# Optimization experiments

Measured on AMD Instinct MI355X. Metric: run time of the kernel, lower is better.

The kernel has to match this reference:

```python
import jax, jax.numpy as jnp
import numpy as np


def setup_inputs() -> dict:
    key = jax.random.key(0)
    kx, ky = jax.random.split(key)
    B, N, M, D = 8, 4096, 4096, 128
    x = jax.random.normal(kx, (B, N, D), dtype=jnp.float32)
    y = jax.random.normal(ky, (B, M, D), dtype=jnp.float32)
    return {"x": x, "y": y}


def reference(x, y):
    # Pairwise L2 distances, equivalent to torch.cdist(x, y) (p=2).
    # ||x_i - y_j||^2 = ||x_i||^2 + ||y_j||^2 - 2 <x_i, y_j>
    x2 = jnp.sum(x * x, axis=-1)[:, :, None]          # [B, N, 1]
    y2 = jnp.sum(y * y, axis=-1)[:, None, :]          # [B, 1, M]
    xy = jnp.einsum("bnd,bmd->bnm", x, y)             # [B, N, M]
    D = jnp.sqrt(jnp.maximum(x2 + y2 - 2.0 * xy, 0.0))  # [B, N, M]
    coverage = D.min(axis=1).mean(axis=-1)            # min over N -> [B, M] -> [B]
    precision = D.min(axis=2).mean(axis=-1)           # min over M -> [B, N] -> [B]
    return (coverage + precision).mean()              # scalar Chamfer loss
```

## Files before the change

kernel.cpp:

```cpp
#include <hip/hip_runtime.h>
#include <cstdint>


#define B_   8
#define N_   4096
#define M_   4096
#define D_   128
#define TPB  8
#define ROWS_PB 256
#define XG   (N_ / ROWS_PB)
#define CHUNKS (M_ / (TPB * 64))

typedef __bf16 bf16x8 __attribute__((ext_vector_type(8)));
typedef float  f32x4  __attribute__((ext_vector_type(4)));
typedef unsigned int u32;

static __device__ __forceinline__ unsigned short f2bf(float f) {
  unsigned u = __float_as_uint(f);
  u += 0x7FFFu + ((u >> 16) & 1u);
  return (unsigned short)(u >> 16);
}

static __device__ __forceinline__ void gld16(void* lds, const void* g) {
  __builtin_amdgcn_global_load_lds(
      (const __attribute__((address_space(1))) void*)g,
      (__attribute__((address_space(3))) void*)lds, 16, 0, 0);
}

__global__ __launch_bounds__(256) void pass1_prep(
    const float* __restrict__ x, const float* __restrict__ y,
    unsigned short* __restrict__ xb, unsigned short* __restrict__ yb,
    float* __restrict__ x2, float* __restrict__ y2)
{
  const int ROWS = B_ * N_;
  int gw   = (blockIdx.x * 256 + threadIdx.x) >> 6;
  int lane = threadIdx.x & 63;
  int half = lane >> 5, sub = lane & 31;
  int row2 = gw * 2 + half;
  bool isx = row2 < ROWS;
  const float* src; unsigned short* dst; float* nrm; int row;
  if (isx) { src = x; dst = xb; nrm = x2; row = row2; }
  else     { src = y; dst = yb; nrm = y2; row = row2 - ROWS; }
  size_t base = (size_t)row * D_ + sub * 4;
  float4 v = *(const float4*)(src + base);
  float sx = isx ? -2.0f : 1.0f;
  u32 p0 = (u32)f2bf(sx * v.x) | ((u32)f2bf(sx * v.y) << 16);
  u32 p1 = (u32)f2bf(sx * v.z) | ((u32)f2bf(sx * v.w) << 16);
  *(uint2*)(dst + base) = make_uint2(p0, p1);
  float s = v.x * v.x + v.y * v.y + v.z * v.z + v.w * v.w;
  #pragma unroll
  for (int m = 1; m < 32; m <<= 1) s += __shfl_xor(s, m, 64);
  if (sub == 0) nrm[row] = s;
}

__global__ __launch_bounds__(256) void pass2_tile(
    const unsigned short* __restrict__ xb, const unsigned short* __restrict__ yb,
    const float* __restrict__ x2, const float* __restrict__ y2,
    float* __restrict__ rowpart, float* __restrict__ colpart)
{
  __shared__ unsigned short ys[2 * 8192];
  __shared__ float cminW[2][16 * 64];

  const int tid  = threadIdx.x;
  const int wave = tid >> 6;
  const int lane = tid & 63;
  const int quad = lane >> 4;
  const int l15  = lane & 15;

  const int id    = blockIdx.x;
  const int b     = id & 7;
  const int xg    = (id >> 3) & 15;
  const int chunk = id >> 7;
  const int n0    = xg * ROWS_PB;
  const int mc0   = chunk * (TPB * 64);

  int srcoff[4], ldsoff[4];
  #pragma unroll
  for (int i = 0; i < 4; ++i) {
    int p  = (wave * 4 + i) * 1024 + lane * 16;
    int r  = p >> 8;
    int pc = (p >> 4) & 15;
    int c  = pc ^ (r & 15);
    srcoff[i] = r * D_ + c * 8;
    ldsoff[i] = (wave * 4 + i) * 1024;
  }

  {
    const unsigned short* src = yb + ((size_t)b * M_ + mc0) * D_;
    #pragma unroll
    for (int i = 0; i < 4; ++i) gld16((char*)ys + ldsoff[i], src + srcoff[i]);
  }

  bf16x8 afrag[4][4];
  const size_t xrow0 = (size_t)b * N_ + n0 + wave * 64;
  #pragma unroll
  for (int kb = 0; kb < 4; ++kb)
    #pragma unroll
    for (int rt = 0; rt < 4; ++rt)
      afrag[kb][rt] = *(const bf16x8*)(xb + (xrow0 + rt * 16 + l15) * D_ + kb * 32 + quad * 8);

  f32x4 xvv[4];
  #pragma unroll
  for (int rt = 0; rt < 4; ++rt)
    #pragma unroll
    for (int r = 0; r < 4; ++r)
      xvv[rt][r] = x2[(size_t)b * N_ + n0 + wave * 64 + rt * 16 + quad * 4 + r];

  const float FINF = __uint_as_float(0x7F800000u);
  float rmin2[4][4];
  #pragma unroll
  for (int rt = 0; rt < 4; ++rt)
    #pragma unroll
    for (int r = 0; r < 4; ++r) rmin2[rt][r] = FINF;

  #pragma unroll 1
  for (int t = 0; t < TPB; ++t) {
    const int m0 = mc0 + t * 64;
    const int d  = (t & 1) * 16384;
    __syncthreads();

    float y2r[4];
    #pragma unroll
    for (int ct = 0; ct < 4; ++ct)
      y2r[ct] = y2[(size_t)b * M_ + m0 + ct * 16 + l15];

    if (t + 1 < TPB) {
      const unsigned short* src = yb + ((size_t)b * M_ + m0 + 64) * D_;
      char* dst = (char*)ys + (16384 - d);
      #pragma unroll
      for (int i = 0; i < 4; ++i) gld16(dst + ldsoff[i], src + srcoff[i]);
    }

    if (t > 0 && tid < 64) {
      const float* cb = cminW[(t - 1) & 1];
      float v = cb[tid];
      #pragma unroll
      for (int w = 1; w < 16; ++w) v = fminf(v, cb[w * 64 + tid]);
      colpart[(size_t)xg * (B_ * M_) + (size_t)b * M_ + (m0 - 64) + tid] = v;
    }

    #pragma unroll
    for (int ct = 0; ct < 4; ++ct) {
      f32x4 a[4];
      #pragma unroll
      for (int rt = 0; rt < 4; ++rt) a[rt] = xvv[rt];
      #pragma unroll
      for (int kb = 0; kb < 4; ++kb) {
        const int row = ct * 16 + l15;
        const int pcB = (kb * 4 + quad) ^ l15;
        bf16x8 bfr = *(const bf16x8*)((const char*)ys + d + row * 256 + pcB * 16);
        #pragma unroll
        for (int rt = 0; rt < 4; ++rt)
          a[rt] = __builtin_amdgcn_mfma_f32_16x16x32_bf16(afrag[kb][rt], bfr, a[rt], 0, 0, 0);
      }
      float yv = y2r[ct];
      float cm = FINF;
      #pragma unroll
      for (int rt = 0; rt < 4; ++rt) {
        #pragma unroll
        for (int r = 0; r < 4; ++r) {
          float s = a[rt][r] + yv;
          rmin2[rt][r] = fminf(rmin2[rt][r], s);
          cm = fminf(cm, s);
        }
      }
      cminW[t & 1][(wave * 4 + quad) * 64 + ct * 16 + l15] = cm;
    }
  }

  __syncthreads();
  if (tid < 64) {
    const float* cb = cminW[(TPB - 1) & 1];
    float v = cb[tid];
    #pragma unroll
    for (int w = 1; w < 16; ++w) v = fminf(v, cb[w * 64 + tid]);
    colpart[(size_t)xg * (B_ * M_) + (size_t)b * M_ + (mc0 + (TPB - 1) * 64) + tid] = v;
  }

  #pragma unroll
  for (int rt = 0; rt < 4; ++rt) {
    #pragma unroll
    for (int r = 0; r < 4; ++r) {
      float v = rmin2[rt][r];
      v = fminf(v, __shfl_xor(v, 1, 64));
      v = fminf(v, __shfl_xor(v, 2, 64));
      v = fminf(v, __shfl_xor(v, 4, 64));
      v = fminf(v, __shfl_xor(v, 8, 64));
      if (l15 == 0)
        rowpart[(size_t)chunk * (B_ * N_) + (size_t)b * N_ + n0 + wave * 64 + rt * 16 + quad * 4 + r] = v;
    }
  }
}

__global__ __launch_bounds__(256) void pass3_final(
    const float* __restrict__ rowpart, const float* __restrict__ colpart,
    float* __restrict__ out)
{
  const int BN = B_ * N_;
  float s1 = 0.0f, s2 = 0.0f;
  for (int i = blockIdx.x * 256 + threadIdx.x; i < BN; i += 64 * 256) {
    float r = rowpart[i];
    #pragma unroll
    for (int c = 1; c < CHUNKS; ++c) r = fminf(r, rowpart[c * BN + i]);
    s1 += sqrtf(fmaxf(r, 0.0f));
    float m = colpart[i];
    #pragma unroll
    for (int g = 1; g < XG; ++g) m = fminf(m, colpart[g * BN + i]);
    s2 += sqrtf(fmaxf(m, 0.0f));
  }
  float s = s1 + s2;
  #pragma unroll
  for (int m = 1; m < 64; m <<= 1) s += __shfl_xor(s, m, 64);
  __shared__ float r1[4];
  int wave = threadIdx.x >> 6, lane = threadIdx.x & 63;
  if (lane == 0) r1[wave] = s;
  __syncthreads();
  if (threadIdx.x == 0)
    atomicAdd(out, (r1[0] + r1[1] + r1[2] + r1[3]) / (float)(B_ * N_));
}

extern "C" void kernel_launch(void* const* d_in, const int* in_sizes, int n_in,
                              void* d_out, int out_size, void* d_ws, size_t ws_size,
                              hipStream_t stream)
{
  const float* x = (const float*)d_in[0];
  const float* y = (const float*)d_in[1];
  char* ws = (char*)d_ws;

  unsigned short* xb = (unsigned short*)(ws);
  unsigned short* yb = (unsigned short*)(ws + (8u << 20));
  float* x2      = (float*)(ws + (16u << 20));
  float* y2      = (float*)(ws + (16u << 20) + (1u << 17));
  float* rowpart = (float*)(ws + (16u << 20) + (2u << 17));
  float* colpart = (float*)(ws + (16u << 20) + (10u << 17));
  float* outf = (float*)d_out;

  hipMemsetAsync(outf, 0, sizeof(float), stream);

  pass1_prep<<<(B_ * N_) / 4, 256, 0, stream>>>(x, y, xb, yb, x2, y2);

  pass2_tile<<<B_ * XG * CHUNKS, 256, 0, stream>>>(xb, yb, x2, y2, rowpart, colpart);

  pass3_final<<<64, 256, 0, stream>>>(rowpart, colpart, outf);
}
```

Baseline: 121.6 us.

## Replace partial-min buffers with global atomicMin and drop LDS column reduction

The row and column minima are now reduced straight into global arrays using integer atomicMin on the float bit patterns. The arrays are initialised to +inf in the prep pass. This removes the LDS cross-wave column-min buffer and its per-tile reduction, and shrinks the final pass from scanning 8 and 16 partial slices down to a single pass. The B fragment loads are also batched ahead of the MFMA block, which is wrapped in s_setprio. The cost is many contended global atomics per column, up to 64 writers per address.

```diff
diff --git a/kernel.cpp b/kernel.cpp
--- a/kernel.cpp
+++ b/kernel.cpp
@@ -30,7 +30,8 @@
 __global__ __launch_bounds__(256) void pass1_prep(
     const float* __restrict__ x, const float* __restrict__ y,
     unsigned short* __restrict__ xb, unsigned short* __restrict__ yb,
-    float* __restrict__ x2, float* __restrict__ y2)
+    float* __restrict__ x2, float* __restrict__ y2,
+    float* __restrict__ rowmin, float* __restrict__ colmin)
 {
   const int ROWS = B_ * N_;
   int gw   = (blockIdx.x * 256 + threadIdx.x) >> 6;
@@ -38,9 +39,9 @@
   int half = lane >> 5, sub = lane & 31;
   int row2 = gw * 2 + half;
   bool isx = row2 < ROWS;
-  const float* src; unsigned short* dst; float* nrm; int row;
-  if (isx) { src = x; dst = xb; nrm = x2; row = row2; }
-  else     { src = y; dst = yb; nrm = y2; row = row2 - ROWS; }
+  const float* src; unsigned short* dst; float* nrm; float* minp; int row;
+  if (isx) { src = x; dst = xb; nrm = x2; minp = rowmin; row = row2; }
+  else     { src = y; dst = yb; nrm = y2; minp = colmin; row = row2 - ROWS; }
   size_t base = (size_t)row * D_ + sub * 4;
   float4 v = *(const float4*)(src + base);
   float sx = isx ? -2.0f : 1.0f;
@@ -50,16 +51,16 @@
   float s = v.x * v.x + v.y * v.y + v.z * v.z + v.w * v.w;
   #pragma unroll
   for (int m = 1; m < 32; m <<= 1) s += __shfl_xor(s, m, 64);
-  if (sub == 0) nrm[row] = s;
+  if (sub == 0)      nrm[row]  = s;
+  else if (sub == 1) minp[row] = __uint_as_float(0x7F800000u);
 }
 
 __global__ __launch_bounds__(256) void pass2_tile(
     const unsigned short* __restrict__ xb, const unsigned short* __restrict__ yb,
     const float* __restrict__ x2, const float* __restrict__ y2,
-    float* __restrict__ rowpart, float* __restrict__ colpart)
+    float* __restrict__ rowmin, float* __restrict__ colmin)
 {
   __shared__ unsigned short ys[2 * 8192];
-  __shared__ float cminW[2][16 * 64];
 
   const int tid  = threadIdx.x;
   const int wave = tid >> 6;
@@ -119,11 +120,6 @@
     const int d  = (t & 1) * 16384;
     __syncthreads();
 
-    float y2r[4];
-    #pragma unroll
-    for (int ct = 0; ct < 4; ++ct)
-      y2r[ct] = y2[(size_t)b * M_ + m0 + ct * 16 + l15];
-
     if (t + 1 < TPB) {
       const unsigned short* src = yb + ((size_t)b * M_ + m0 + 64) * D_;
       char* dst = (char*)ys + (16384 - d);
@@ -131,50 +127,48 @@
       for (int i = 0; i < 4; ++i) gld16(dst + ldsoff[i], src + srcoff[i]);
     }
 
-    if (t > 0 && tid < 64) {
-      const float* cb = cminW[(t - 1) & 1];
-      float v = cb[tid];
-      #pragma unroll
-      for (int w = 1; w < 16; ++w) v = fminf(v, cb[w * 64 + tid]);
-      colpart[(size_t)xg * (B_ * M_) + (size_t)b * M_ + (m0 - 64) + tid] = v;
-    }
+    float y2r[4];
+    #pragma unroll
+    for (int ct = 0; ct < 4; ++ct)
+      y2r[ct] = y2[(size_t)b * M_ + m0 + ct * 16 + l15];
 
     #pragma unroll
     for (int ct = 0; ct < 4; ++ct) {
-      f32x4 a[4];
-      #pragma unroll
-      for (int rt = 0; rt < 4; ++rt) a[rt] = xvv[rt];
+      bf16x8 bfr[4];
       #pragma unroll
       for (int kb = 0; kb < 4; ++kb) {
         const int row = ct * 16 + l15;
         const int pcB = (kb * 4 + quad) ^ l15;
-        bf16x8 bfr = *(const bf16x8*)((const char*)ys + d + row * 256 + pcB * 16);
+        bfr[kb] = *(const bf16x8*)((const char*)ys + d + row * 256 + pcB * 16);
+      }
+      f32x4 a[4];
+      #pragma unroll
+      for (int rt = 0; rt < 4; ++rt) a[rt] = xvv[rt];
+      __builtin_amdgcn_s_setprio(1);
+      #pragma unroll
+      for (int kb = 0; kb < 4; ++kb)
         #pragma unroll
         for (int rt = 0; rt < 4; ++rt)
-          a[rt] = __builtin_amdgcn_mfma_f32_16x16x32_bf16(afrag[kb][rt], bfr, a[rt], 0, 0, 0);
+          a[rt] = __builtin_amdgcn_mfma_f32_16x16x32_bf16(afrag[kb][rt], bfr[kb], a[rt], 0, 0, 0);
+      __builtin_amdgcn_s_setprio(0);
+
+      float yv = y2r[ct];
+      float c[4];
+      #pragma unroll
+      for (int rt = 0; rt < 4; ++rt) {
+        float s0 = a[rt][0] + yv; rmin2[rt][0] = fminf(rmin2[rt][0], s0);
+        float s1 = a[rt][1] + yv; rmin2[rt][1] = fminf(rmin2[rt][1], s1);
+        float s2 = a[rt][2] + yv; rmin2[rt][2] = fminf(rmin2[rt][2], s2);
+        float s3 = a[rt][3] + yv; rmin2[rt][3] = fminf(rmin2[rt][3], s3);
+        c[rt] = fminf(fminf(s0, s1), fminf(s2, s3));
       }
-      float yv = y2r[ct];
-      float cm = FINF;
-      #pragma unroll
-      for (int rt = 0; rt < 4; ++rt) {
-        #pragma unroll
-        for (int r = 0; r < 4; ++r) {
-          float s = a[rt][r] + yv;
-          rmin2[rt][r] = fminf(rmin2[rt][r], s);
-          cm = fminf(cm, s);
-        }
-      }
-      cminW[t & 1][(wave * 4 + quad) * 64 + ct * 16 + l15] = cm;
+      float cm = fminf(fminf(c[0], c[1]), fminf(c[2], c[3]));
+      cm = fminf(cm, __shfl_xor(cm, 16, 64));
+      cm = fminf(cm, __shfl_xor(cm, 32, 64));
+      if (quad == 0)
+        atomicMin((int*)(colmin + (size_t)b * M_ + m0 + ct * 16 + l15),
+                  __float_as_int(cm));
     }
-  }
-
-  __syncthreads();
-  if (tid < 64) {
-    const float* cb = cminW[(TPB - 1) & 1];
-    float v = cb[tid];
-    #pragma unroll
-    for (int w = 1; w < 16; ++w) v = fminf(v, cb[w * 64 + tid]);
-    colpart[(size_t)xg * (B_ * M_) + (size_t)b * M_ + (mc0 + (TPB - 1) * 64) + tid] = v;
   }
 
   #pragma unroll
@@ -187,26 +181,21 @@
       v = fminf(v, __shfl_xor(v, 4, 64));
       v = fminf(v, __shfl_xor(v, 8, 64));
       if (l15 == 0)
-        rowpart[(size_t)chunk * (B_ * N_) + (size_t)b * N_ + n0 + wave * 64 + rt * 16 + quad * 4 + r] = v;
+        atomicMin((int*)(rowmin + (size_t)b * N_ + n0 + wave * 64 + rt * 16 + quad * 4 + r),
+                  __float_as_int(v));
     }
   }
 }
 
 __global__ __launch_bounds__(256) void pass3_final(
-    const float* __restrict__ rowpart, const float* __restrict__ colpart,
+    const float* __restrict__ rowmin, const float* __restrict__ colmin,
     float* __restrict__ out)
 {
   const int BN = B_ * N_;
   float s1 = 0.0f, s2 = 0.0f;
   for (int i = blockIdx.x * 256 + threadIdx.x; i < BN; i += 64 * 256) {
-    float r = rowpart[i];
-    #pragma unroll
-    for (int c = 1; c < CHUNKS; ++c) r = fminf(r, rowpart[c * BN + i]);
-    s1 += sqrtf(fmaxf(r, 0.0f));
-    float m = colpart[i];
-    #pragma unroll
-    for (int g = 1; g < XG; ++g) m = fminf(m, colpart[g * BN + i]);
-    s2 += sqrtf(fmaxf(m, 0.0f));
+    s1 += sqrtf(fmaxf(rowmin[i], 0.0f));
+    s2 += sqrtf(fmaxf(colmin[i], 0.0f));
   }
   float s = s1 + s2;
   #pragma unroll
@@ -229,17 +218,17 @@
 
   unsigned short* xb = (unsigned short*)(ws);
   unsigned short* yb = (unsigned short*)(ws + (8u << 20));
-  float* x2      = (float*)(ws + (16u << 20));
-  float* y2      = (float*)(ws + (16u << 20) + (1u << 17));
-  float* rowpart = (float*)(ws + (16u << 20) + (2u << 17));
-  float* colpart = (float*)(ws + (16u << 20) + (10u << 17));
+  float* x2     = (float*)(ws + (16u << 20));
+  float* y2     = (float*)(ws + (16u << 20) + (1u << 17));
+  float* rowmin = (float*)(ws + (16u << 20) + (2u << 17));
+  float* colmin = (float*)(ws + (16u << 20) + (3u << 17));
   float* outf = (float*)d_out;
 
   hipMemsetAsync(outf, 0, sizeof(float), stream);
 
-  pass1_prep<<<(B_ * N_) / 4, 256, 0, stream>>>(x, y, xb, yb, x2, y2);
-
-  pass2_tile<<<B_ * XG * CHUNKS, 256, 0, stream>>>(xb, yb, x2, y2, rowpart, colpart);
-
-  pass3_final<<<64, 256, 0, stream>>>(rowpart, colpart, outf);
-}
+  pass1_prep<<<(B_ * N_) / 4, 256, 0, stream>>>(x, y, xb, yb, x2, y2, rowmin, colmin);
+
+  pass2_tile<<<B_ * XG * CHUNKS, 256, 0, stream>>>(xb, yb, x2, y2, rowmin, colmin);
+
+  pass3_final<<<64, 256, 0, stream>>>(rowmin, colmin, outf);
+}
```

New measurement: 127.6 us. 1.05x slower.

## Fuse bf16 conversion and norm computation into tile kernel, drop prep pass

Applied to the files above, without the earlier changes.

Removes the separate prep kernel. The tile kernel now loads fp32 x and y directly, converts them to bf16 in registers, computes the squared norms on the fly, and writes the y tiles into swizzled LDS. The next y tile is prefetched through registers in two halves interleaved between MFMA column tiles, replacing the global_load_lds path. Column-min partials are pre-reduced with a shuffle, which halves the cminW reduction. This removes one launch and the bf16 workspace round trip, but each x row block and y chunk is now converted redundantly by many blocks, and more VALU and register work sits inside the main loop.

```diff
diff --git a/kernel.cpp b/kernel.cpp
--- a/kernel.cpp
+++ b/kernel.cpp
@@ -10,6 +10,7 @@
 #define ROWS_PB 256
 #define XG   (N_ / ROWS_PB)
 #define CHUNKS (M_ / (TPB * 64))
+#define GRID (B_ * XG * CHUNKS)
 
 typedef __bf16 bf16x8 __attribute__((ext_vector_type(8)));
 typedef float  f32x4  __attribute__((ext_vector_type(4)));
@@ -20,52 +21,56 @@
   u += 0x7FFFu + ((u >> 16) & 1u);
   return (unsigned short)(u >> 16);
 }
-
-static __device__ __forceinline__ void gld16(void* lds, const void* g) {
-  __builtin_amdgcn_global_load_lds(
-      (const __attribute__((address_space(1))) void*)g,
-      (__attribute__((address_space(3))) void*)lds, 16, 0, 0);
-}
-
-__global__ __launch_bounds__(256) void pass1_prep(
+static __device__ __forceinline__ u32 pk2(float a, float b) {
+  return (u32)f2bf(a) | ((u32)f2bf(b) << 16);
+}
+
+
+#define DO_CT(CT)                                                              \
+  {                                                                            \
+    f32x4 a[4];                                                                \
+    _Pragma("unroll")                                                          \
+    for (int rt = 0; rt < 4; ++rt) a[rt] = xvv[rt];                            \
+    _Pragma("unroll")                                                          \
+    for (int kb = 0; kb < 4; ++kb) {                                           \
+      const int row = (CT) * 16 + l15;                                         \
+      const int pcB = (kb * 4 + quad) ^ l15;                                   \
+      bf16x8 bfr = *(const bf16x8*)((const char*)ys + d + row * 256 + pcB * 16); \
+      _Pragma("unroll")                                                        \
+      for (int rt = 0; rt < 4; ++rt)                                           \
+        a[rt] = __builtin_amdgcn_mfma_f32_16x16x32_bf16(afrag[kb][rt], bfr, a[rt], 0, 0, 0); \
+    }                                                                          \
+    float yv = y2r[(CT)];                                                      \
+    float cm = FINF;                                                           \
+    _Pragma("unroll")                                                          \
+    for (int rt = 0; rt < 4; ++rt) {                                           \
+      _Pragma("unroll")                                                        \
+      for (int r = 0; r < 4; ++r) {                                            \
+        float s = a[rt][r] + yv;                                               \
+        rmin2[rt][r] = fminf(rmin2[rt][r], s);                                 \
+        cm = fminf(cm, s);                                                     \
+      }                                                                        \
+    }                                                                          \
+    cm = fminf(cm, __shfl_xor(cm, 16, 64));               \
+    if ((quad & 1) == 0)                                                       \
+      cminW[t & 1][wave * 2 + (quad >> 1)][(CT) * 16 + l15] = cm;              \
+  }
+
+__global__ __launch_bounds__(256) void tile_fused(
     const float* __restrict__ x, const float* __restrict__ y,
-    unsigned short* __restrict__ xb, unsigned short* __restrict__ yb,
-    float* __restrict__ x2, float* __restrict__ y2)
-{
-  const int ROWS = B_ * N_;
-  int gw   = (blockIdx.x * 256 + threadIdx.x) >> 6;
-  int lane = threadIdx.x & 63;
-  int half = lane >> 5, sub = lane & 31;
-  int row2 = gw * 2 + half;
-  bool isx = row2 < ROWS;
-  const float* src; unsigned short* dst; float* nrm; int row;
-  if (isx) { src = x; dst = xb; nrm = x2; row = row2; }
-  else     { src = y; dst = yb; nrm = y2; row = row2 - ROWS; }
-  size_t base = (size_t)row * D_ + sub * 4;
-  float4 v = *(const float4*)(src + base);
-  float sx = isx ? -2.0f : 1.0f;
-  u32 p0 = (u32)f2bf(sx * v.x) | ((u32)f2bf(sx * v.y) << 16);
-  u32 p1 = (u32)f2bf(sx * v.z) | ((u32)f2bf(sx * v.w) << 16);
-  *(uint2*)(dst + base) = make_uint2(p0, p1);
-  float s = v.x * v.x + v.y * v.y + v.z * v.z + v.w * v.w;
-  #pragma unroll
-  for (int m = 1; m < 32; m <<= 1) s += __shfl_xor(s, m, 64);
-  if (sub == 0) nrm[row] = s;
-}
-
-__global__ __launch_bounds__(256) void pass2_tile(
-    const unsigned short* __restrict__ xb, const unsigned short* __restrict__ yb,
-    const float* __restrict__ x2, const float* __restrict__ y2,
     float* __restrict__ rowpart, float* __restrict__ colpart)
 {
   __shared__ unsigned short ys[2 * 8192];
-  __shared__ float cminW[2][16 * 64];
+  __shared__ float ys2[2][64];
+  __shared__ float cminW[2][8][64];
 
   const int tid  = threadIdx.x;
   const int wave = tid >> 6;
   const int lane = tid & 63;
   const int quad = lane >> 4;
   const int l15  = lane & 15;
+  const int r0   = tid >> 2;
+  const int qp   = tid & 3;
 
   const int id    = blockIdx.x;
   const int b     = id & 7;
@@ -74,37 +79,61 @@
   const int n0    = xg * ROWS_PB;
   const int mc0   = chunk * (TPB * 64);
 
-  int srcoff[4], ldsoff[4];
-  #pragma unroll
-  for (int i = 0; i < 4; ++i) {
-    int p  = (wave * 4 + i) * 1024 + lane * 16;
-    int r  = p >> 8;
-    int pc = (p >> 4) & 15;
-    int c  = pc ^ (r & 15);
-    srcoff[i] = r * D_ + c * 8;
-    ldsoff[i] = (wave * 4 + i) * 1024;
-  }
-
   {
-    const unsigned short* src = yb + ((size_t)b * M_ + mc0) * D_;
-    #pragma unroll
-    for (int i = 0; i < 4; ++i) gld16((char*)ys + ldsoff[i], src + srcoff[i]);
+    const float* ysrc = y + (size_t)(b * M_ + mc0 + r0) * D_ + qp * 32;
+    float4 v0[8];
+    #pragma unroll
+    for (int i = 0; i < 8; ++i) v0[i] = *(const float4*)(ysrc + i * 4);
+    float p = 0.0f;
+    #pragma unroll
+    for (int i = 0; i < 8; ++i)
+      p += v0[i].x*v0[i].x + v0[i].y*v0[i].y + v0[i].z*v0[i].z + v0[i].w*v0[i].w;
+    p += __shfl_xor(p, 1, 64);
+    p += __shfl_xor(p, 2, 64);
+    if ((lane & 3) == 0) ys2[0][r0] = p;
+    #pragma unroll
+    for (int j = 0; j < 4; ++j) {
+      int pc = (qp * 4 + j) ^ (r0 & 15);
+      uint4 w;
+      w.x = pk2(v0[2*j].x,   v0[2*j].y);
+      w.y = pk2(v0[2*j].z,   v0[2*j].w);
+      w.z = pk2(v0[2*j+1].x, v0[2*j+1].y);
+      w.w = pk2(v0[2*j+1].z, v0[2*j+1].w);
+      *(uint4*)((char*)ys + r0 * 256 + pc * 16) = w;
+    }
   }
 
   bf16x8 afrag[4][4];
-  const size_t xrow0 = (size_t)b * N_ + n0 + wave * 64;
-  #pragma unroll
-  for (int kb = 0; kb < 4; ++kb)
+  f32x4 xvv[4];
+  {
+    float x2row[4];
+    #pragma unroll
+    for (int rt = 0; rt < 4; ++rt) {
+      const float* xs = x + (size_t)(b * N_ + n0 + wave * 64 + rt * 16 + l15) * D_ + quad * 8;
+      float p = 0.0f;
+      #pragma unroll
+      for (int kb = 0; kb < 4; ++kb) {
+        float4 u0 = *(const float4*)(xs + kb * 32);
+        float4 u1 = *(const float4*)(xs + kb * 32 + 4);
+        p += u0.x*u0.x + u0.y*u0.y + u0.z*u0.z + u0.w*u0.w
+           + u1.x*u1.x + u1.y*u1.y + u1.z*u1.z + u1.w*u1.w;
+        union { u32 w[4]; bf16x8 v; } tt;
+        tt.w[0] = pk2(-2.f*u0.x, -2.f*u0.y);
+        tt.w[1] = pk2(-2.f*u0.z, -2.f*u0.w);
+        tt.w[2] = pk2(-2.f*u1.x, -2.f*u1.y);
+        tt.w[3] = pk2(-2.f*u1.z, -2.f*u1.w);
+        afrag[kb][rt] = tt.v;
+      }
+      p += __shfl_xor(p, 16, 64);
+      p += __shfl_xor(p, 32, 64);
+      x2row[rt] = p;
+    }
     #pragma unroll
     for (int rt = 0; rt < 4; ++rt)
-      afrag[kb][rt] = *(const bf16x8*)(xb + (xrow0 + rt * 16 + l15) * D_ + kb * 32 + quad * 8);
-
-  f32x4 xvv[4];
-  #pragma unroll
-  for (int rt = 0; rt < 4; ++rt)
-    #pragma unroll
-    for (int r = 0; r < 4; ++r)
-      xvv[rt][r] = x2[(size_t)b * N_ + n0 + wave * 64 + rt * 16 + quad * 4 + r];
+      #pragma unroll
+      for (int r = 0; r < 4; ++r)
+        xvv[rt][r] = __shfl(x2row[rt], quad * 4 + r, 16);
+  }
 
   const float FINF = __uint_as_float(0x7F800000u);
   float rmin2[4][4];
@@ -113,67 +142,88 @@
     #pragma unroll
     for (int r = 0; r < 4; ++r) rmin2[rt][r] = FINF;
 
+  __syncthreads();
+
   #pragma unroll 1
   for (int t = 0; t < TPB; ++t) {
     const int m0 = mc0 + t * 64;
     const int d  = (t & 1) * 16384;
+    const int dn = 16384 - d;
+    const bool pf = (t + 1 < TPB);
+    const float* nsrc = y + (size_t)(b * M_ + m0 + 64 + r0) * D_ + qp * 32;
+
+    float4 sv[4];
+    if (pf) {
+      #pragma unroll
+      for (int i = 0; i < 4; ++i) sv[i] = *(const float4*)(nsrc + i * 4);
+    }
+
+    if (t > 0 && tid < 64) {
+      const float* cb = &cminW[(t - 1) & 1][0][0];
+      float v = cb[tid];
+      #pragma unroll
+      for (int w = 1; w < 8; ++w) v = fminf(v, cb[w * 64 + tid]);
+      colpart[(size_t)xg * (B_ * M_) + (size_t)b * M_ + (m0 - 64) + tid] = v;
+    }
+
+    float y2r[4];
+    #pragma unroll
+    for (int ct = 0; ct < 4; ++ct) y2r[ct] = ys2[t & 1][ct * 16 + l15];
+
+    float y2p = 0.0f;
+
+    DO_CT(0)
+    DO_CT(1)
+
+    if (pf) {
+      #pragma unroll
+      for (int i = 0; i < 4; ++i)
+        y2p += sv[i].x*sv[i].x + sv[i].y*sv[i].y + sv[i].z*sv[i].z + sv[i].w*sv[i].w;
+      #pragma unroll
+      for (int j = 0; j < 2; ++j) {
+        int pc = (qp * 4 + j) ^ (r0 & 15);
+        uint4 w;
+        w.x = pk2(sv[2*j].x,   sv[2*j].y);
+        w.y = pk2(sv[2*j].z,   sv[2*j].w);
+        w.z = pk2(sv[2*j+1].x, sv[2*j+1].y);
+        w.w = pk2(sv[2*j+1].z, sv[2*j+1].w);
+        *(uint4*)((char*)ys + dn + r0 * 256 + pc * 16) = w;
+      }
+      #pragma unroll
+      for (int i = 0; i < 4; ++i) sv[i] = *(const float4*)(nsrc + 16 + i * 4);
+    }
+
+    DO_CT(2)
+    DO_CT(3)
+
+    if (pf) {
+      #pragma unroll
+      for (int i = 0; i < 4; ++i)
+        y2p += sv[i].x*sv[i].x + sv[i].y*sv[i].y + sv[i].z*sv[i].z + sv[i].w*sv[i].w;
+      #pragma unroll
+      for (int j = 2; j < 4; ++j) {
+        int pc = (qp * 4 + j) ^ (r0 & 15);
+        int i0 = 2 * (j - 2);
+        uint4 w;
+        w.x = pk2(sv[i0].x,   sv[i0].y);
+        w.y = pk2(sv[i0].z,   sv[i0].w);
+        w.z = pk2(sv[i0+1].x, sv[i0+1].y);
+        w.w = pk2(sv[i0+1].z, sv[i0+1].w);
+        *(uint4*)((char*)ys + dn + r0 * 256 + pc * 16) = w;
+      }
+      y2p += __shfl_xor(y2p, 1, 64);
+      y2p += __shfl_xor(y2p, 2, 64);
+      if ((lane & 3) == 0) ys2[(t + 1) & 1][r0] = y2p;
+    }
+
     __syncthreads();
-
-    float y2r[4];
-    #pragma unroll
-    for (int ct = 0; ct < 4; ++ct)
-      y2r[ct] = y2[(size_t)b * M_ + m0 + ct * 16 + l15];
-
-    if (t + 1 < TPB) {
-      const unsigned short* src = yb + ((size_t)b * M_ + m0 + 64) * D_;
-      char* dst = (char*)ys + (16384 - d);
-      #pragma unroll
-      for (int i = 0; i < 4; ++i) gld16(dst + ldsoff[i], src + srcoff[i]);
-    }
-
-    if (t > 0 && tid < 64) {
-      const float* cb = cminW[(t - 1) & 1];
-      float v = cb[tid];
-      #pragma unroll
-      for (int w = 1; w < 16; ++w) v = fminf(v, cb[w * 64 + tid]);
-      colpart[(size_t)xg * (B_ * M_) + (size_t)b * M_ + (m0 - 64) + tid] = v;
-    }
-
-    #pragma unroll
-    for (int ct = 0; ct < 4; ++ct) {
-      f32x4 a[4];
-      #pragma unroll
-      for (int rt = 0; rt < 4; ++rt) a[rt] = xvv[rt];
-      #pragma unroll
-      for (int kb = 0; kb < 4; ++kb) {
-        const int row = ct * 16 + l15;
-        const int pcB = (kb * 4 + quad) ^ l15;
-        bf16x8 bfr = *(const bf16x8*)((const char*)ys + d + row * 256 + pcB * 16);
-        #pragma unroll
-        for (int rt = 0; rt < 4; ++rt)
-          a[rt] = __builtin_amdgcn_mfma_f32_16x16x32_bf16(afrag[kb][rt], bfr, a[rt], 0, 0, 0);
-      }
-      float yv = y2r[ct];
-      float cm = FINF;
-      #pragma unroll
-      for (int rt = 0; rt < 4; ++rt) {
-        #pragma unroll
-        for (int r = 0; r < 4; ++r) {
-          float s = a[rt][r] + yv;
-          rmin2[rt][r] = fminf(rmin2[rt][r], s);
-          cm = fminf(cm, s);
-        }
-      }
-      cminW[t & 1][(wave * 4 + quad) * 64 + ct * 16 + l15] = cm;
-    }
-  }
-
-  __syncthreads();
+  }
+
   if (tid < 64) {
-    const float* cb = cminW[(TPB - 1) & 1];
+    const float* cb = &cminW[(TPB - 1) & 1][0][0];
     float v = cb[tid];
     #pragma unroll
-    for (int w = 1; w < 16; ++w) v = fminf(v, cb[w * 64 + tid]);
+    for (int w = 1; w < 8; ++w) v = fminf(v, cb[w * 64 + tid]);
     colpart[(size_t)xg * (B_ * M_) + (size_t)b * M_ + (mc0 + (TPB - 1) * 64) + tid] = v;
   }
 
@@ -227,19 +277,13 @@
   const float* y = (const float*)d_in[1];
   char* ws = (char*)d_ws;
 
-  unsigned short* xb = (unsigned short*)(ws);
-  unsigned short* yb = (unsigned short*)(ws + (8u << 20));
-  float* x2      = (float*)(ws + (16u << 20));
-  float* y2      = (float*)(ws + (16u << 20) + (1u << 17));
-  float* rowpart = (float*)(ws + (16u << 20) + (2u << 17));
-  float* colpart = (float*)(ws + (16u << 20) + (10u << 17));
+  float* rowpart = (float*)(ws);
+  float* colpart = (float*)(ws + (1u << 20));
   float* outf = (float*)d_out;
 
   hipMemsetAsync(outf, 0, sizeof(float), stream);
 
-  pass1_prep<<<(B_ * N_) / 4, 256, 0, stream>>>(x, y, xb, yb, x2, y2);
-
-  pass2_tile<<<B_ * XG * CHUNKS, 256, 0, stream>>>(xb, yb, x2, y2, rowpart, colpart);
+  tile_fused<<<GRID, 256, 0, stream>>>(x, y, rowpart, colpart);
 
   pass3_final<<<64, 256, 0, stream>>>(rowpart, colpart, outf);
 }
```

Result: slower. 142.6 us (+17.3%).
